# Kernel tuning notes

Hardware: AMD Instinct MI355X
Metric: run time of the kernel (lower is better)

The kernel has to match this reference:

```python
import jax, jax.numpy as jnp
import numpy as np

ON_OFF = "off"  # init kwarg: 'off' includes the next-frame temporal candidate

def setup_inputs() -> dict:
    key = jax.random.key(0)
    k1, k2 = jax.random.split(key)
    xs = jax.random.normal(k1, (4, 32, 128, 32), dtype=jnp.float32)  # [B,T,N,D]
    A = jax.random.randint(k2, (1, 128, 128), 0, 2, dtype=jnp.int32)  # [1,N,N] adjacency
    return {"xs": xs, "A": A}

def reference(xs, A):
    B, T, N, D = xs.shape
    # A_f = A + I ; neighbors are nonzero entries (self-loop included via eye)
    A_f = A[0].astype(xs.dtype) + jnp.eye(N, dtype=xs.dtype)
    spatial_mask = A_f != 0  # [N,N] : spatial_mask[n, j] -> j is neighbor of n

    # Candidate set per (frame t, node n): prev-frame self, next-frame self (on_off=='off'),
    # and all spatial neighbors at frame t. Padded to fixed size K = N + 2 with masks.
    spat = jnp.broadcast_to(xs[:, :, None, :, :], (B, T, N, N, D))   # [B,T,N,N,D]
    prev = jnp.concatenate([xs[:, :1], xs[:, :-1]], axis=1)          # [B,T,N,D] (t=0 masked)
    nxt = jnp.concatenate([xs[:, 1:], xs[:, -1:]], axis=1)           # [B,T,N,D] (t=T-1 masked)
    cand = jnp.concatenate([prev[:, :, :, None, :], nxt[:, :, :, None, :], spat], axis=3)  # [B,T,N,N+2,D]

    t = jnp.arange(T)
    prev_m = jnp.broadcast_to((t > 0)[:, None, None], (T, N, 1))
    if ON_OFF == "off":
        next_m = jnp.broadcast_to((t < T - 1)[:, None, None], (T, N, 1))
    else:
        next_m = jnp.zeros((T, N, 1), dtype=bool)
    sp_m = jnp.broadcast_to(spatial_mask[None], (T, N, N))
    mask = jnp.concatenate([prev_m, next_m, sp_m], axis=2)  # [T,N,N+2]

    # Masked median = torch.median semantics (lower median): sort with +inf padding,
    # pick index (k-1)//2 where k = number of valid candidates.
    vals = jnp.where(mask[None, :, :, :, None], cand, jnp.inf)
    vals = jnp.sort(vals, axis=3)
    k = mask.sum(axis=2)              # [T,N]
    med_idx = (k - 1) // 2            # lower median index
    idx = jnp.broadcast_to(med_idx[None, :, :, None, None], (B, T, N, 1, D))
    ys = jnp.take_along_axis(vals, idx, axis=3)[:, :, :, 0, :]  # [B,T,N,D]
    return ys
```

## Files before the change

kernel.cpp:

```cpp
#include <hip/hip_runtime.h>
#include <stdint.h>
#include <math.h>

#define BB 4
#define TT 32
#define NN 128
#define DD 32
#define NPB 16
#define TPB (NPB * DD)
#define NBLK (BB * TT * (NN / NPB))
#define CAP 16
#define SSTR (TPB + 4)

#define SID_PREV 0xFEu
#define SID_NEXT 0xFFu

__device__ __forceinline__ int bin8(float x) {
    int i = (int)fmaf(x, 5.0f, 4.0f);
    i = i < 0 ? 0 : i;
    return i > 7 ? 7 : i;
}

__global__ __launch_bounds__(TPB) void median_kernel(const float* __restrict__ xs,
                                                     const int* __restrict__ A,
                                                     float* __restrict__ out) {
    __shared__ float sval[NN * DD];
    __shared__ uint8_t sbin[NN * DD];
    __shared__ uint32_t snbr_w[NPB * NN / 4];
    __shared__ int sdeg[NPB];
    __shared__ uint8_t slist[(CAP + 1) * SSTR];

    const int tid = threadIdx.x;
    const int bid = blockIdx.x;
    const int g = ((bid & 7) << 7) | (bid >> 3);
    const int ng = g & (NN / NPB - 1);
    const int t  = (g >> 3) & (TT - 1);
    const int b  = g >> 8;
    const int n0 = ng * NPB;

    const int d = tid & (DD - 1);
    const int nl = tid >> 5;
    const int n = n0 + nl;
    const int pv = (t > 0) ? 1 : 0;
    const int nv = (t < TT - 1) ? 1 : 0;
    const int ne = pv + nv;

    float exv0 = 0.0f, exv1 = 0.0f;
    if (pv) exv0 = xs[(((size_t)(b * TT + t - 1) * NN) + n) * DD + d];
    if (nv) {
        float v = xs[(((size_t)(b * TT + t + 1) * NN) + n) * DD + d];
        if (pv) exv1 = v; else exv0 = v;
    }

    const float4* src4 = (const float4*)(xs + ((size_t)(b * TT + t) * NN) * DD);
    #pragma unroll
    for (int s = 0; s < 2; ++s) {
        int i4 = tid + (s << 9);
        float4 f = src4[i4];
        ((float4*)sval)[i4] = f;
        uint32_t pk = (uint32_t)bin8(f.x) | ((uint32_t)bin8(f.y) << 8)
                    | ((uint32_t)bin8(f.z) << 16) | ((uint32_t)bin8(f.w) << 24);
        ((uint32_t*)sbin)[i4] = pk;
    }

    {
        uint8_t* snbr = (uint8_t*)snbr_w;
        const int lane = tid & 63;
        const int wid = tid >> 6;
        const unsigned long long lmask = (1ULL << lane) - 1ULL;
        #pragma unroll
        for (int h = 0; h < 2; ++h) {
            const int rr = wid * 2 + h;
            const int nrow = n0 + rr;
            const int* arow = A + nrow * NN;
            const bool b0 = (arow[lane] != 0) || (lane == nrow);
            const bool b1 = (arow[lane + 64] != 0) || (lane + 64 == nrow);
            const unsigned long long m0 = __ballot(b0);
            const unsigned long long m1 = __ballot(b1);
            const int c0 = __popcll(m0);
            if (b0) snbr[rr * NN + __popcll(m0 & lmask)] = (uint8_t)lane;
            if (b1) snbr[rr * NN + c0 + __popcll(m1 & lmask)] = (uint8_t)(lane + 64);
            if (lane == 0) sdeg[rr] = c0 + __popcll(m1);
        }
    }
    __syncthreads();

    const int dg = sdeg[nl];
    const int k = dg + ne;
    const uint32_t r = (uint32_t)((k - 1) >> 1);
    const uint8_t* nb = (const uint8_t*)snbr_w + nl * NN;
    const float INFV = __uint_as_float(0x7F800000u);

    auto gbin = [&](uint32_t id) -> int { return (int)sbin[id * DD + d]; };
    const int be0 = bin8(exv0);
    const int be1 = bin8(exv1);

    unsigned long long pcnt = 0ull;
    {
        int j = 0;
        for (; j + 8 <= dg; j += 8) {
            uint32_t nw0 = *(const uint32_t*)(nb + j);
            uint32_t nw1 = *(const uint32_t*)(nb + j + 4);
            int bsv[8];
            #pragma unroll
            for (int q = 0; q < 4; ++q) {
                bsv[q]     = gbin((nw0 >> (q * 8)) & 0xFFu);
                bsv[q + 4] = gbin((nw1 >> (q * 8)) & 0xFFu);
            }
            #pragma unroll
            for (int q = 0; q < 8; ++q) pcnt += 1ull << (bsv[q] * 8);
        }
        for (; j < dg; ++j) pcnt += 1ull << (gbin(nb[j]) * 8);
        if (ne >= 1) pcnt += 1ull << (be0 * 8);
        if (ne == 2) pcnt += 1ull << (be1 * 8);
    }

    uint32_t cum = 0, lowcnt = 0, mexp = 0;
    int selbin = -1;
    #pragma unroll
    for (int bb = 0; bb < 8; ++bb) {
        uint32_t bc = (uint32_t)(pcnt >> (bb * 8)) & 0xFFu;
        uint32_t nc = cum + bc;
        if (selbin < 0 && r < nc) { selbin = bb; lowcnt = cum; mexp = bc; }
        cum = nc;
    }
    const bool fb = (mexp > CAP);
    const uint32_t rp = r - lowcnt;
    const int storebin = fb ? -1 : selbin;

    int mc = 0;
    {
        int j = 0;
        for (; j + 8 <= dg; j += 8) {
            uint32_t nw0 = *(const uint32_t*)(nb + j);
            uint32_t nw1 = *(const uint32_t*)(nb + j + 4);
            uint32_t ids[8]; int bsv[8];
            #pragma unroll
            for (int q = 0; q < 4; ++q) {
                ids[q]     = (nw0 >> (q * 8)) & 0xFFu;
                ids[q + 4] = (nw1 >> (q * 8)) & 0xFFu;
            }
            #pragma unroll
            for (int q = 0; q < 8; ++q) bsv[q] = gbin(ids[q]);
            #pragma unroll
            for (int q = 0; q < 8; ++q) {
                int slot = mc > CAP ? CAP : mc;
                slist[slot * SSTR + tid] = (uint8_t)ids[q];
                mc += (bsv[q] == storebin);
            }
        }
        for (; j < dg; ++j) {
            uint32_t id = nb[j];
            int bv = gbin(id);
            int slot = mc > CAP ? CAP : mc;
            slist[slot * SSTR + tid] = (uint8_t)id;
            mc += (bv == storebin);
        }
        if (ne >= 1) {
            int slot = mc > CAP ? CAP : mc;
            slist[slot * SSTR + tid] = (uint8_t)SID_PREV;
            mc += (be0 == storebin);
        }
        if (ne == 2) {
            int slot = mc > CAP ? CAP : mc;
            slist[slot * SSTR + tid] = (uint8_t)SID_NEXT;
            mc += (be1 == storebin);
        }
    }

    auto bandval = [&](int e) -> float {
        uint32_t id = slist[e * SSTR + tid];
        float v = sval[(id & 127u) * DD + d];
        v = (id == SID_PREV) ? exv0 : v;
        v = (id == SID_NEXT) ? exv1 : v;
        return v;
    };

    float ki[CAP];
    uint32_t cn[CAP];
    #pragma unroll
    for (int u = 0; u < CAP; ++u) {
        float v = bandval(u);
        ki[u] = (u < mc) ? v : INFV;
        cn[u] = 0;
    }
    int mm = mc;
    #pragma unroll
    for (int off = 32; off; off >>= 1) {
        int o = __shfl_xor(mm, off);
        mm = mm > o ? mm : o;
    }
    {
        int j = 0;
        for (; j + 2 <= mm; j += 2) {
            float x0 = bandval(j);
            float x1 = bandval(j + 1);
            x0 = (j < mc) ? x0 : INFV;
            x1 = (j + 1 < mc) ? x1 : INFV;
            #pragma unroll
            for (int u = 0; u < CAP; ++u) cn[u] += (x0 < ki[u]) + (x1 < ki[u]);
        }
        if (j < mm) {
            float x = bandval(j);
            x = (j < mc) ? x : INFV;
            #pragma unroll
            for (int u = 0; u < CAP; ++u) cn[u] += (x < ki[u]);
        }
    }
    float result = 0.0f;
    bool found = fb;
    #pragma unroll
    for (int u = 0; u < CAP; ++u) {
        if (!found && u < mc && cn[u] == rp) { result = ki[u]; found = true; }
    }

    if (__ballot(!found)) {
        uint32_t eq[CAP];
        #pragma unroll
        for (int u = 0; u < CAP; ++u) eq[u] = 0;
        for (int j = 0; j < mm; ++j) {
            float x = bandval(j);
            x = (j < mc) ? x : INFV;
            #pragma unroll
            for (int u = 0; u < CAP; ++u) eq[u] += (x == ki[u]);
        }
        #pragma unroll
        for (int u = 0; u < CAP; ++u) {
            if (!found && u < mc && cn[u] <= rp && rp < cn[u] + eq[u]) {
                result = ki[u]; found = true;
            }
        }
    }

    if (__ballot(fb)) {
        bool done = !fb;
        for (int i0 = 0; __ballot(!done && i0 < k); i0 += 8) {
            float k8[8]; uint32_t c8[8];
            #pragma unroll
            for (int u = 0; u < 8; ++u) {
                int i = i0 + u;
                float sv = sval[nb[i & 127] * DD + d];
                float ev = ((i - dg) == 0) ? exv0 : exv1;
                float v = (i < dg) ? sv : ev;
                k8[u] = (i < k) ? v : INFV;
                c8[u] = 0;
            }
            for (int j = 0; j < dg; ++j) {
                float xv = sval[nb[j] * DD + d];
                #pragma unroll
                for (int u = 0; u < 8; ++u) c8[u] += (xv < k8[u]);
            }
            if (ne >= 1) {
                #pragma unroll
                for (int u = 0; u < 8; ++u) c8[u] += (exv0 < k8[u]);
            }
            if (ne == 2) {
                #pragma unroll
                for (int u = 0; u < 8; ++u) c8[u] += (exv1 < k8[u]);
            }
            #pragma unroll
            for (int u = 0; u < 8; ++u) {
                if (!done && (i0 + u) < k && c8[u] == r) { result = k8[u]; done = true; }
            }
        }
        if (__ballot(!done)) {
            for (int i0 = 0; __ballot(!done && i0 < k); i0 += 4) {
                float k4[4]; uint32_t lt4[4], le4[4];
                #pragma unroll
                for (int u = 0; u < 4; ++u) {
                    int i = i0 + u;
                    float sv = sval[nb[i & 127] * DD + d];
                    float ev = ((i - dg) == 0) ? exv0 : exv1;
                    float v = (i < dg) ? sv : ev;
                    k4[u] = (i < k) ? v : INFV;
                    lt4[u] = 0; le4[u] = 0;
                }
                for (int j = 0; j < dg; ++j) {
                    float xv = sval[nb[j] * DD + d];
                    #pragma unroll
                    for (int u = 0; u < 4; ++u) { lt4[u] += (xv < k4[u]); le4[u] += (xv <= k4[u]); }
                }
                if (ne >= 1) {
                    #pragma unroll
                    for (int u = 0; u < 4; ++u) { lt4[u] += (exv0 < k4[u]); le4[u] += (exv0 <= k4[u]); }
                }
                if (ne == 2) {
                    #pragma unroll
                    for (int u = 0; u < 4; ++u) { lt4[u] += (exv1 < k4[u]); le4[u] += (exv1 <= k4[u]); }
                }
                #pragma unroll
                for (int u = 0; u < 4; ++u) {
                    if (!done && (i0 + u) < k && lt4[u] <= r && r < le4[u]) {
                        result = k4[u]; done = true;
                    }
                }
            }
        }
    }

    out[(((size_t)(b * TT + t) * NN) + n) * DD + d] = result;
}

extern "C" void kernel_launch(void* const* d_in, const int* in_sizes, int n_in,
                              void* d_out, int out_size, void* d_ws, size_t ws_size,
                              hipStream_t stream) {
    const float* xs = (const float*)d_in[0];
    const int* A = (const int*)d_in[1];
    float* out = (float*)d_out;
    (void)d_ws; (void)ws_size;

    median_kernel<<<NBLK, TPB, 0, stream>>>(xs, A, out);
}
```

Measured before the change: 121.3 us.

## Replace per-neighbor bin histogram loop with bitset popcount over adjacency masks

Builds per-bin, per-feature bitsets over all 128 nodes in shared memory, stores each row's adjacency as a 128-bit mask, and computes the 8-bin histogram with AND plus popcount instead of walking every neighbor. This removes the data-dependent gather loop of about 64 neighbors per thread. In exchange it adds a bitset-building pass over shared memory and one more block barrier, plus a little extra shared memory.

```diff
diff --git a/kernel.cpp b/kernel.cpp
--- a/kernel.cpp
+++ b/kernel.cpp
@@ -26,7 +26,9 @@
                                                      float* __restrict__ out) {
     __shared__ float sval[NN * DD];
     __shared__ uint8_t sbin[NN * DD];
+    __shared__ __align__(16) uint32_t sbit[8 * DD * 4];
     __shared__ uint32_t snbr_w[NPB * NN / 4];
+    __shared__ __align__(16) uint32_t smask[NPB][4];
     __shared__ int sdeg[NPB];
     __shared__ uint8_t slist[(CAP + 1) * SSTR];
 
@@ -80,8 +82,31 @@
             const int c0 = __popcll(m0);
             if (b0) snbr[rr * NN + __popcll(m0 & lmask)] = (uint8_t)lane;
             if (b1) snbr[rr * NN + c0 + __popcll(m1 & lmask)] = (uint8_t)(lane + 64);
-            if (lane == 0) sdeg[rr] = c0 + __popcll(m1);
-        }
+            if (lane == 0) {
+                sdeg[rr] = c0 + __popcll(m1);
+                smask[rr][0] = (uint32_t)m0;
+                smask[rr][1] = (uint32_t)(m0 >> 32);
+                smask[rr][2] = (uint32_t)m1;
+                smask[rr][3] = (uint32_t)(m1 >> 32);
+            }
+        }
+    }
+    __syncthreads();
+
+    {
+        const int rep = tid >> 7;
+        const int wo  = (tid >> 5) & 3;
+        const int dd  = tid & 31;
+        const int ba = rep * 2, bc = ba + 1;
+        uint32_t lo = 0u, hi = 0u;
+        #pragma unroll 8
+        for (int q = 0; q < 32; ++q) {
+            const int bv = (int)sbin[(wo * 32 + q) * DD + dd];
+            lo |= (bv == ba) ? (1u << q) : 0u;
+            hi |= (bv == bc) ? (1u << q) : 0u;
+        }
+        sbit[ba * 128 + dd * 4 + wo] = lo;
+        sbit[bc * 128 + dd * 4 + wo] = hi;
     }
     __syncthreads();
 
@@ -95,31 +120,22 @@
     const int be0 = bin8(exv0);
     const int be1 = bin8(exv1);
 
-    unsigned long long pcnt = 0ull;
-    {
-        int j = 0;
-        for (; j + 8 <= dg; j += 8) {
-            uint32_t nw0 = *(const uint32_t*)(nb + j);
-            uint32_t nw1 = *(const uint32_t*)(nb + j + 4);
-            int bsv[8];
-            #pragma unroll
-            for (int q = 0; q < 4; ++q) {
-                bsv[q]     = gbin((nw0 >> (q * 8)) & 0xFFu);
-                bsv[q + 4] = gbin((nw1 >> (q * 8)) & 0xFFu);
-            }
-            #pragma unroll
-            for (int q = 0; q < 8; ++q) pcnt += 1ull << (bsv[q] * 8);
-        }
-        for (; j < dg; ++j) pcnt += 1ull << (gbin(nb[j]) * 8);
-        if (ne >= 1) pcnt += 1ull << (be0 * 8);
-        if (ne == 2) pcnt += 1ull << (be1 * 8);
+    const uint4 am4 = *((const uint4*)smask[nl]);
+    int hist[8];
+    const uint4* sbit4 = (const uint4*)sbit;
+    #pragma unroll
+    for (int bb = 0; bb < 8; ++bb) {
+        uint4 w = sbit4[bb * 32 + d];
+        hist[bb] = __popc(w.x & am4.x) + __popc(w.y & am4.y)
+                 + __popc(w.z & am4.z) + __popc(w.w & am4.w);
     }
 
     uint32_t cum = 0, lowcnt = 0, mexp = 0;
     int selbin = -1;
     #pragma unroll
     for (int bb = 0; bb < 8; ++bb) {
-        uint32_t bc = (uint32_t)(pcnt >> (bb * 8)) & 0xFFu;
+        uint32_t bc = (uint32_t)hist[bb] + ((ne >= 1 && be0 == bb) ? 1u : 0u)
+                                         + ((ne == 2 && be1 == bb) ? 1u : 0u);
         uint32_t nc = cum + bc;
         if (selbin < 0 && r < nc) { selbin = bb; lowcnt = cum; mexp = bc; }
         cum = nc;
```

Result: no change. 120.6 us (-0.5%).
